# Performance work log

Measured on AMD Instinct MI355X. Metric: run time of the kernel, lower is better.

## Reference

```python
import jax, jax.numpy as jnp
import numpy as np

PERIOD = 24
TREND_WINDOW = 24
HALF = TREND_WINDOW // 2          # 12
DROP = (TREND_WINDOW - 1) // 2    # 11 rows dropped off the batch axis (as in original)


def setup_inputs() -> dict:
    key = jax.random.key(0)
    x = jax.random.normal(key, (4096, 2048), dtype=jnp.float32)
    return {"x": x}


def _trend(x):
    # Centered moving average with boundary-clipped (variable-size) windows,
    # vectorized via an exclusive cumulative sum.  x: (B, T)
    B, T = x.shape
    cs = jnp.concatenate([jnp.zeros((B, 1), x.dtype), jnp.cumsum(x, axis=1)], axis=1)  # (B, T+1)
    i = jnp.arange(T)
    start = jnp.clip(i - HALF, 0, T)           # max(0, i - half_window)
    end = jnp.clip(i + HALF + 1, 0, T)         # min(T, i + half_window + 1)
    sums = cs[:, end] - cs[:, start]           # (B, T)
    counts = (end - start).astype(x.dtype)     # (T,)
    return sums / counts


def _seasonal(x):
    # Phase-wise mean: seasonal[b, t] = mean_{t' : t' % PERIOD == t % PERIOD} x[b, t']
    B, T = x.shape
    phase = jnp.arange(T) % PERIOD                                    # (T,)
    sums = jax.ops.segment_sum(x.T, phase, num_segments=PERIOD)      # (P, B)
    counts = jax.ops.segment_sum(jnp.ones((T,), x.dtype), phase, num_segments=PERIOD)  # (P,)
    means = sums / counts[:, None]                                    # (P, B)
    return means[phase].T                                             # (B, T)


def reference(x):
    trend = _trend(x)
    detrended = x - trend                 # additive method
    seasonal = _seasonal(detrended)
    residual = x - trend - seasonal
    out = jnp.stack([trend, seasonal, residual], axis=2)  # (B, T, 3)
    # drop_na: original slices along the batch axis
    return out[DROP:, :, :]
```

## Files before the change

kernel.cpp:

```cpp
#include <hip/hip_runtime.h>

#define TT 2048
#define BB 4096
#define DROP_ROWS 11
#define PERIOD 24
#define BLOCK 256
#define HALF 12
#define WAVES (BLOCK / 64)

__global__ __launch_bounds__(BLOCK) void seasonal_decomp_kernel(
    const float* __restrict__ x, float* __restrict__ out) {
  __shared__ float buf[6144];
  __shared__ float wt0[WAVES], wt1[WAVES];
  __shared__ float pp[PERIOD][8];
  __shared__ float pmean[PERIOD];
  float* const sd = buf;
  float* const cs = buf + 2048;
  float* const sout = buf;

  const int tid = threadIdx.x;
  const int lane = tid & 63;
  const int wave = tid >> 6;
  const int row = blockIdx.x + DROP_ROWS;

  const float4* rx = (const float4*)(x + (size_t)row * TT);
  float4 v0 = rx[tid];
  float4 v1 = rx[tid + 256];

  float s0 = v0.x + v0.y + v0.z + v0.w;
  float s1 = v1.x + v1.y + v1.z + v1.w;
  float i0 = s0, i1 = s1;
  #pragma unroll
  for (int off = 1; off < 64; off <<= 1) {
    float t0 = __shfl_up(i0, off, 64);
    float t1 = __shfl_up(i1, off, 64);
    if (lane >= off) { i0 += t0; i1 += t1; }
  }
  if (lane == 63) { wt0[wave] = i0; wt1[wave] = i1; }
  __syncthreads();
  float W0 = 0.f, W1 = 0.f, H = 0.f;
  #pragma unroll
  for (int w = 0; w < WAVES; ++w) {
    float a = wt0[w], b = wt1[w];
    H += a;
    if (w < wave) { W0 += a; W1 += b; }
  }
  const float P0 = W0 + (i0 - s0);
  const float P1 = H + W1 + (i1 - s1);

  float4 c0, c1;
  c0.x = P0; c0.y = P0 + v0.x; c0.z = c0.y + v0.y; c0.w = c0.z + v0.z;
  c1.x = P1; c1.y = P1 + v1.x; c1.z = c1.y + v1.y; c1.w = c1.z + v1.z;
  ((float4*)cs)[tid] = c0;
  ((float4*)cs)[tid + 256] = c1;
  if (tid == 255) cs[TT] = P1 + s1;
  __syncthreads();

  float tr[8], sdr[8];
  #pragma unroll
  for (int j = 0; j < 8; ++j) {
    int t = tid + 256 * j;
    int s = t - HALF; if (s < 0) s = 0;
    int e = t + HALF + 1; if (e > TT) e = TT;
    float wsum = cs[e] - cs[s];
    float xt = cs[t + 1] - cs[t];
    tr[j] = wsum / (float)(e - s);
    sdr[j] = xt - tr[j];
    sd[t] = sdr[j];
  }
  __syncthreads();

  if (tid < PERIOD * 8) {
    int p = tid >> 3;
    int j = tid & 7;
    int cnt = (p < 8) ? 86 : 85;
    float s = 0.f;
    for (int m = j; m < cnt; m += 8) s += sd[p + PERIOD * m];
    pp[p][j] = s;
  }
  __syncthreads();
  if (tid < PERIOD) {
    float s = 0.f;
    #pragma unroll
    for (int j = 0; j < 8; ++j) s += pp[tid][j];
    pmean[tid] = s / ((tid < 8) ? 86.f : 85.f);
  }
  __syncthreads();

  #pragma unroll
  for (int j = 0; j < 8; ++j) {
    int t = tid + 256 * j;
    float sea = pmean[t % PERIOD];
    sout[3 * t]     = tr[j];
    sout[3 * t + 1] = sea;
    sout[3 * t + 2] = sdr[j] - sea;
  }
  __syncthreads();
  float4* orow = (float4*)(out + (size_t)blockIdx.x * (TT * 3));
  const float4* so4 = (const float4*)sout;
  #pragma unroll
  for (int j = 0; j < 6; ++j) orow[tid + 256 * j] = so4[tid + 256 * j];
}

extern "C" void kernel_launch(void* const* d_in, const int* in_sizes, int n_in,
                              void* d_out, int out_size, void* d_ws, size_t ws_size,
                              hipStream_t stream) {
  const float* x = (const float*)d_in[0];
  float* out = (float*)d_out;
  seasonal_decomp_kernel<<<BB - DROP_ROWS, BLOCK, 0, stream>>>(x, out);
}
```

Measured before the change: 27.36 us.

## Recompute trend from prefix sums and write interleaved output directly from registers

Drops the large shared staging buffer for detrended values and interleaved output. The trend and detrended values are now recomputed from the shared prefix-sum array both in the phase reduction and in the output pass, and each thread assembles its float4 of interleaved (trend, seasonal, residual) directly before storing. Divisions are replaced with a small reciprocal table and constant reciprocals. This cuts shared memory per block from about 24KB to about 8KB and removes two barriers, which should raise occupancy, at the cost of redundant shared loads and arithmetic. The reciprocal multiply can differ slightly from true division.

```diff
diff --git a/kernel.cpp b/kernel.cpp
--- a/kernel.cpp
+++ b/kernel.cpp
@@ -10,18 +10,18 @@
 
 __global__ __launch_bounds__(BLOCK) void seasonal_decomp_kernel(
     const float* __restrict__ x, float* __restrict__ out) {
-  __shared__ float buf[6144];
+  __shared__ float cs[TT + 1];
+  __shared__ float rc[32];
   __shared__ float wt0[WAVES], wt1[WAVES];
   __shared__ float pp[PERIOD][8];
   __shared__ float pmean[PERIOD];
-  float* const sd = buf;
-  float* const cs = buf + 2048;
-  float* const sout = buf;
 
   const int tid = threadIdx.x;
   const int lane = tid & 63;
   const int wave = tid >> 6;
   const int row = blockIdx.x + DROP_ROWS;
+
+  if (tid < 32) rc[tid] = 1.0f / (float)(tid ? tid : 1);
 
   const float4* rx = (const float4*)(x + (size_t)row * TT);
   float4 v0 = rx[tid];
@@ -56,26 +56,19 @@
   if (tid == 255) cs[TT] = P1 + s1;
   __syncthreads();
 
-  float tr[8], sdr[8];
-  #pragma unroll
-  for (int j = 0; j < 8; ++j) {
-    int t = tid + 256 * j;
-    int s = t - HALF; if (s < 0) s = 0;
-    int e = t + HALF + 1; if (e > TT) e = TT;
-    float wsum = cs[e] - cs[s];
-    float xt = cs[t + 1] - cs[t];
-    tr[j] = wsum / (float)(e - s);
-    sdr[j] = xt - tr[j];
-    sd[t] = sdr[j];
-  }
-  __syncthreads();
-
   if (tid < PERIOD * 8) {
     int p = tid >> 3;
     int j = tid & 7;
     int cnt = (p < 8) ? 86 : 85;
     float s = 0.f;
-    for (int m = j; m < cnt; m += 8) s += sd[p + PERIOD * m];
+    for (int m = j; m < cnt; m += 8) {
+      int t = p + PERIOD * m;
+      int a = t - HALF; if (a < 0) a = 0;
+      int e = t + HALF + 1; if (e > TT) e = TT;
+      float tr = (cs[e] - cs[a]) * rc[e - a];
+      float xt = cs[t + 1] - cs[t];
+      s += xt - tr;
+    }
     pp[p][j] = s;
   }
   __syncthreads();
@@ -83,23 +76,43 @@
     float s = 0.f;
     #pragma unroll
     for (int j = 0; j < 8; ++j) s += pp[tid][j];
-    pmean[tid] = s / ((tid < 8) ? 86.f : 85.f);
+    pmean[tid] = s * ((tid < 8) ? (1.0f / 86.0f) : (1.0f / 85.0f));
   }
   __syncthreads();
 
+  float4* orow = (float4*)(out + (size_t)blockIdx.x * (TT * 3));
   #pragma unroll
-  for (int j = 0; j < 8; ++j) {
-    int t = tid + 256 * j;
-    float sea = pmean[t % PERIOD];
-    sout[3 * t]     = tr[j];
-    sout[3 * t + 1] = sea;
-    sout[3 * t + 2] = sdr[j] - sea;
+  for (int j = 0; j < 6; ++j) {
+    int g = tid + 256 * j;
+    int f0 = 4 * g;
+    int t0 = f0 / 3;
+    int r = f0 - 3 * t0;
+    float tr0, se0, re0, tr1, se1, re1;
+    {
+      int t = t0;
+      int a = t - HALF; if (a < 0) a = 0;
+      int e = t + HALF + 1; if (e > TT) e = TT;
+      tr0 = (cs[e] - cs[a]) * rc[e - a];
+      float xt = cs[t + 1] - cs[t];
+      se0 = pmean[t % PERIOD];
+      re0 = xt - tr0 - se0;
+    }
+    {
+      int t = t0 + 1;
+      int a = t - HALF; if (a < 0) a = 0;
+      int e = t + HALF + 1; if (e > TT) e = TT;
+      tr1 = (cs[e] - cs[a]) * rc[e - a];
+      float xt = cs[t + 1] - cs[t];
+      se1 = pmean[t % PERIOD];
+      re1 = xt - tr1 - se1;
+    }
+    float4 v;
+    v.x = (r == 0) ? tr0 : ((r == 1) ? se0 : re0);
+    v.y = (r == 0) ? se0 : ((r == 1) ? re0 : tr1);
+    v.z = (r == 0) ? re0 : ((r == 1) ? tr1 : se1);
+    v.w = (r == 0) ? tr1 : ((r == 1) ? se1 : re1);
+    orow[g] = v;
   }
-  __syncthreads();
-  float4* orow = (float4*)(out + (size_t)blockIdx.x * (TT * 3));
-  const float4* so4 = (const float4*)sout;
-  #pragma unroll
-  for (int j = 0; j < 6; ++j) orow[tid + 256 * j] = so4[tid + 256 * j];
 }
 
 extern "C" void kernel_launch(void* const* d_in, const int* in_sizes, int n_in,
```

Measured after the change: 27.62 us. Within noise of the previous version (+0.9%).

## Process four rows per block and prefetch next row's input during compute

Applied to the files above, without the earlier changes.

Each block now handles four consecutive output rows in a loop instead of one. The next row's global loads are issued before the intermediate barrier so they overlap with the current row's trend and seasonal computation. The kernel also replaces the interior-window divide with a multiply by 1/25, uses reciprocal multiplies for the phase means, and computes the phase index incrementally. The grid shrinks fourfold, which lowers parallelism and serializes rows inside each block, and adds more barriers per block.

```diff
diff --git a/kernel.cpp b/kernel.cpp
--- a/kernel.cpp
+++ b/kernel.cpp
@@ -3,103 +3,141 @@
 #define TT 2048
 #define BB 4096
 #define DROP_ROWS 11
+#define NOUT (BB - DROP_ROWS)
 #define PERIOD 24
 #define BLOCK 256
 #define HALF 12
-#define WAVES (BLOCK / 64)
+#define ROWS 4
 
 __global__ __launch_bounds__(BLOCK) void seasonal_decomp_kernel(
     const float* __restrict__ x, float* __restrict__ out) {
   __shared__ float buf[6144];
-  __shared__ float wt0[WAVES], wt1[WAVES];
+  __shared__ float wt0[4], wt1[4];
   __shared__ float pp[PERIOD][8];
   __shared__ float pmean[PERIOD];
-  float* const sd = buf;
-  float* const cs = buf + 2048;
+  float* const cs = buf;
+  float* const sd = buf + 2080;
   float* const sout = buf;
 
   const int tid = threadIdx.x;
   const int lane = tid & 63;
   const int wave = tid >> 6;
-  const int row = blockIdx.x + DROP_ROWS;
+  const int rbase = blockIdx.x * ROWS;
 
-  const float4* rx = (const float4*)(x + (size_t)row * TT);
-  float4 v0 = rx[tid];
-  float4 v1 = rx[tid + 256];
+  float4 v0, v1;
+  if (rbase < NOUT) {
+    const float4* rx = (const float4*)(x + (size_t)(rbase + DROP_ROWS) * TT);
+    v0 = rx[tid];
+    v1 = rx[tid + 256];
+  }
 
-  float s0 = v0.x + v0.y + v0.z + v0.w;
-  float s1 = v1.x + v1.y + v1.z + v1.w;
-  float i0 = s0, i1 = s1;
-  #pragma unroll
-  for (int off = 1; off < 64; off <<= 1) {
-    float t0 = __shfl_up(i0, off, 64);
-    float t1 = __shfl_up(i1, off, 64);
-    if (lane >= off) { i0 += t0; i1 += t1; }
+  for (int r = 0; r < ROWS; ++r) {
+    const int orow_i = rbase + r;
+    const bool active = (orow_i < NOUT);
+
+    float s0 = 0.f, s1 = 0.f, i0 = 0.f, i1 = 0.f;
+    float tr[8], sdr[8];
+
+    if (active) {
+      s0 = v0.x + v0.y + v0.z + v0.w;
+      s1 = v1.x + v1.y + v1.z + v1.w;
+      i0 = s0; i1 = s1;
+      #pragma unroll
+      for (int off = 1; off < 64; off <<= 1) {
+        float t0 = __shfl_up(i0, off, 64);
+        float t1 = __shfl_up(i1, off, 64);
+        if (lane >= off) { i0 += t0; i1 += t1; }
+      }
+      if (lane == 63) { wt0[wave] = i0; wt1[wave] = i1; }
+    }
+    __syncthreads();
+
+    if (active) {
+      float W0 = 0.f, W1 = 0.f, H = 0.f;
+      #pragma unroll
+      for (int w = 0; w < 4; ++w) {
+        float a = wt0[w], b = wt1[w];
+        H += a;
+        if (w < wave) { W0 += a; W1 += b; }
+      }
+      const float P0 = W0 + (i0 - s0);
+      const float P1 = H + W1 + (i1 - s1);
+      float4 c0, c1;
+      c0.x = P0; c0.y = P0 + v0.x; c0.z = c0.y + v0.y; c0.w = c0.z + v0.z;
+      c1.x = P1; c1.y = P1 + v1.x; c1.z = c1.y + v1.y; c1.w = c1.z + v1.z;
+      ((float4*)cs)[tid] = c0;
+      ((float4*)cs)[tid + 256] = c1;
+      if (tid == 255) cs[TT] = P1 + s1;
+    }
+
+    if (r + 1 < ROWS && rbase + r + 1 < NOUT) {
+      const float4* rx =
+          (const float4*)(x + (size_t)(rbase + r + 1 + DROP_ROWS) * TT);
+      v0 = rx[tid];
+      v1 = rx[tid + 256];
+    }
+    __syncthreads();
+
+    if (active) {
+      #pragma unroll
+      for (int j = 0; j < 8; ++j) {
+        const int t = tid + 256 * j;
+        const float* p = &cs[t];
+        const float xt = p[1] - p[0];
+        float trv;
+        if (t >= HALF && t < TT - HALF - 1) {
+          const float* q = &cs[t - HALF];
+          trv = (q[2 * HALF + 1] - q[0]) * (1.0f / 25.0f);
+        } else {
+          const int a = (t - HALF < 0) ? 0 : t - HALF;
+          const int e = (t + HALF + 1 > TT) ? TT : t + HALF + 1;
+          trv = (cs[e] - cs[a]) / (float)(e - a);
+        }
+        tr[j] = trv;
+        sdr[j] = xt - trv;
+        sd[t] = sdr[j];
+      }
+    }
+    __syncthreads();
+
+    if (active && tid < PERIOD * 8) {
+      const int p = tid >> 3, jj = tid & 7;
+      const int cnt = (p < 8) ? 86 : 85;
+      float s = 0.f;
+      for (int m = jj; m < cnt; m += 8) s += sd[p + PERIOD * m];
+      pp[p][jj] = s;
+    }
+    __syncthreads();
+
+    if (active && tid < PERIOD) {
+      float s = 0.f;
+      #pragma unroll
+      for (int j2 = 0; j2 < 8; ++j2) s += pp[tid][j2];
+      pmean[tid] = s * ((tid < 8) ? (1.0f / 86.f) : (1.0f / 85.f));
+    }
+    __syncthreads();
+
+    if (active) {
+      int ph = tid % PERIOD;
+      #pragma unroll
+      for (int j = 0; j < 8; ++j) {
+        const int t = tid + 256 * j;
+        const float pm = pmean[ph];
+        ph += 16; if (ph >= PERIOD) ph -= PERIOD;
+        sout[3 * t]     = tr[j];
+        sout[3 * t + 1] = pm;
+        sout[3 * t + 2] = sdr[j] - pm;
+      }
+    }
+    __syncthreads();
+
+    if (active) {
+      float4* orow = (float4*)(out + (size_t)orow_i * (TT * 3));
+      const float4* so4 = (const float4*)sout;
+      #pragma unroll
+      for (int j = 0; j < 6; ++j) orow[tid + 256 * j] = so4[tid + 256 * j];
+    }
   }
-  if (lane == 63) { wt0[wave] = i0; wt1[wave] = i1; }
-  __syncthreads();
-  float W0 = 0.f, W1 = 0.f, H = 0.f;
-  #pragma unroll
-  for (int w = 0; w < WAVES; ++w) {
-    float a = wt0[w], b = wt1[w];
-    H += a;
-    if (w < wave) { W0 += a; W1 += b; }
-  }
-  const float P0 = W0 + (i0 - s0);
-  const float P1 = H + W1 + (i1 - s1);
-
-  float4 c0, c1;
-  c0.x = P0; c0.y = P0 + v0.x; c0.z = c0.y + v0.y; c0.w = c0.z + v0.z;
-  c1.x = P1; c1.y = P1 + v1.x; c1.z = c1.y + v1.y; c1.w = c1.z + v1.z;
-  ((float4*)cs)[tid] = c0;
-  ((float4*)cs)[tid + 256] = c1;
-  if (tid == 255) cs[TT] = P1 + s1;
-  __syncthreads();
-
-  float tr[8], sdr[8];
-  #pragma unroll
-  for (int j = 0; j < 8; ++j) {
-    int t = tid + 256 * j;
-    int s = t - HALF; if (s < 0) s = 0;
-    int e = t + HALF + 1; if (e > TT) e = TT;
-    float wsum = cs[e] - cs[s];
-    float xt = cs[t + 1] - cs[t];
-    tr[j] = wsum / (float)(e - s);
-    sdr[j] = xt - tr[j];
-    sd[t] = sdr[j];
-  }
-  __syncthreads();
-
-  if (tid < PERIOD * 8) {
-    int p = tid >> 3;
-    int j = tid & 7;
-    int cnt = (p < 8) ? 86 : 85;
-    float s = 0.f;
-    for (int m = j; m < cnt; m += 8) s += sd[p + PERIOD * m];
-    pp[p][j] = s;
-  }
-  __syncthreads();
-  if (tid < PERIOD) {
-    float s = 0.f;
-    #pragma unroll
-    for (int j = 0; j < 8; ++j) s += pp[tid][j];
-    pmean[tid] = s / ((tid < 8) ? 86.f : 85.f);
-  }
-  __syncthreads();
-
-  #pragma unroll
-  for (int j = 0; j < 8; ++j) {
-    int t = tid + 256 * j;
-    float sea = pmean[t % PERIOD];
-    sout[3 * t]     = tr[j];
-    sout[3 * t + 1] = sea;
-    sout[3 * t + 2] = sdr[j] - sea;
-  }
-  __syncthreads();
-  float4* orow = (float4*)(out + (size_t)blockIdx.x * (TT * 3));
-  const float4* so4 = (const float4*)sout;
-  #pragma unroll
-  for (int j = 0; j < 6; ++j) orow[tid + 256 * j] = so4[tid + 256 * j];
 }
 
 extern "C" void kernel_launch(void* const* d_in, const int* in_sizes, int n_in,
@@ -107,5 +145,6 @@
                               hipStream_t stream) {
   const float* x = (const float*)d_in[0];
   float* out = (float*)d_out;
-  seasonal_decomp_kernel<<<BB - DROP_ROWS, BLOCK, 0, stream>>>(x, out);
+  const int grid = (NOUT + ROWS - 1) / ROWS;
+  seasonal_decomp_kernel<<<grid, BLOCK, 0, stream>>>(x, out);
 }
```

New measurement: 27.58 us. No clear change (+0.8%).
